# Performance work log

Hardware: AMD Instinct MI355X
Metric: run time of the kernel (lower is better)

The kernel has to match this reference:

```python
import jax, jax.numpy as jnp
import numpy as np

# dims from init_kwargs
B, T = 64, 128
CB, DB = 8, 256
IN_DIM = CB + DB            # 264
H_STATE = 512
NUM_HEADS = 4
NUM_SHIFT = 3
M = 128                     # memory content size (slot width)
A = 2048                    # number of memory addresses
READ_SIZE = NUM_HEADS * M   # 512
PARAMS_PER_HEAD = M + 1 + 1 + NUM_SHIFT + 1 + 2 * M  # key,beta,g,shift,gamma,erase,add = 390
UPDATE_SIZE = NUM_HEADS * PARAMS_PER_HEAD             # 1560
EPS = 1e-8


def setup_inputs() -> dict:
    key = jax.random.key(0)
    ks = jax.random.split(key, 4)
    w = lambda k, sh: jax.random.normal(k, sh, jnp.float32) * 0.02
    return {
        "x": jax.random.normal(ks[0], (B, T, IN_DIM), jnp.float32),
        "W_state": w(ks[1], (IN_DIM + H_STATE + READ_SIZE, H_STATE)),
        "b_state": jnp.zeros((H_STATE,), jnp.float32),
        "W_out": w(ks[2], (H_STATE, DB)),
        "b_out": jnp.zeros((DB,), jnp.float32),
        "W_upd": w(ks[3], (H_STATE, UPDATE_SIZE)),
        "b_upd": jnp.zeros((UPDATE_SIZE,), jnp.float32),
    }


def _ntm_step(params, carry, x_t):
    W_state, b_state, W_out, b_out, W_upd, b_upd = params
    h, wt, mem = carry  # h [B,S], wt [B,H,A], mem [B,M,A]

    # --- read from memory with previous attention ---
    read = jnp.einsum('bma,bha->bhm', mem, wt).reshape(B, READ_SIZE)

    # --- controller ---
    ctrl_in = jnp.concatenate([x_t, h, read], axis=-1)
    h_new = jax.nn.sigmoid(ctrl_in @ W_state + b_state)
    out = jax.nn.sigmoid(h_new @ W_out + b_out)
    upd = (h_new @ W_upd + b_upd).reshape(B, NUM_HEADS, PARAMS_PER_HEAD)

    # --- split interface parameters per head ---
    k_vec = upd[..., :M]                                              # key [B,H,M]
    beta = jax.nn.softplus(upd[..., M:M + 1])                         # key strength
    g = jax.nn.sigmoid(upd[..., M + 1:M + 2])                         # interpolation gate
    shift = jax.nn.softmax(upd[..., M + 2:M + 2 + NUM_SHIFT], axis=-1)
    gamma = 1.0 + jax.nn.softplus(upd[..., M + 2 + NUM_SHIFT:M + 3 + NUM_SHIFT])
    erase = jax.nn.sigmoid(upd[..., M + 3 + NUM_SHIFT:2 * M + 3 + NUM_SHIFT])
    add = jnp.tanh(upd[..., 2 * M + 3 + NUM_SHIFT:])

    # --- content addressing: cosine similarity + sharpened softmax ---
    dots = jnp.einsum('bhm,bma->bha', k_vec, mem)
    k_norm = jnp.linalg.norm(k_vec, axis=-1, keepdims=True)           # [B,H,1]
    m_norm = jnp.linalg.norm(mem, axis=1)[:, None, :]                 # [B,1,A]
    sim = dots / (k_norm * m_norm + EPS)
    wc = jax.nn.softmax(beta * sim, axis=-1)

    # --- gate with previous attention ---
    wg = g * wc + (1.0 - g) * wt

    # --- circular convolutional shift (small fixed loop over NUM_SHIFT) ---
    center = NUM_SHIFT // 2
    shifted = jnp.stack([jnp.roll(wg, s - center, axis=-1) for s in range(NUM_SHIFT)], axis=2)  # [B,H,S,A]
    ws = jnp.einsum('bhs,bhsa->bha', shift, shifted)

    # --- sharpening ---
    wp = jnp.power(ws + EPS, gamma)
    wt_new = wp / jnp.sum(wp, axis=-1, keepdims=True)

    # --- memory erase / add ---
    erase_term = jnp.prod(1.0 - jnp.einsum('bhm,bha->bhma', erase, wt_new), axis=1)  # [B,M,A]
    add_term = jnp.einsum('bhm,bha->bma', add, wt_new)
    mem_new = mem * erase_term + add_term

    return (h_new, wt_new, mem_new), out


def reference(x, W_state, b_state, W_out, b_out, W_upd, b_upd):
    # init_state (matches torch module): h=ones, wt one-hot at address 0, mem=0.01
    h0 = jnp.ones((B, H_STATE), jnp.float32)
    wt0 = jnp.zeros((B, NUM_HEADS, A), jnp.float32).at[:, :, 0].set(1.0)
    mem0 = jnp.full((B, M, A), 0.01, jnp.float32)
    params = (W_state, b_state, W_out, b_out, W_upd, b_upd)

    def step(carry, x_t):
        return _ntm_step(params, carry, x_t)

    _, outs = jax.lax.scan(step, (h0, wt0, mem0), jnp.swapaxes(x, 0, 1))
    return jnp.swapaxes(outs, 0, 1)  # [B, T, DB]
```

## Files before the change

kernel.cpp:

```cpp
#include <hip/hip_runtime.h>
#include <math.h>

#define BB 64
#define TT 128
#define DBX 256
#define IND 264
#define HS 512
#define NH 4
#define MMM 128
#define AAA 2048
#define PPH 390
#define NCOLS (DBX + NH*PPH)
#define KTOT (IND + HS + HS)
#define KSPL 8
#define KCH  161
#define EPSF 1e-8f

__device__ __forceinline__ float sigmf(float x){ return 1.0f/(1.0f+expf(-x)); }
__device__ __forceinline__ float softplusf(float x){ return (x > 20.0f) ? x : log1pf(expf(x)); }

__global__ void k_init(float* __restrict__ hT, float* __restrict__ readT,
                       float* __restrict__ wt, float* __restrict__ mem){
  int i = blockIdx.x*blockDim.x + threadIdx.x;
  int stride = gridDim.x*blockDim.x;
  for (int idx=i; idx<BB*MMM*AAA; idx+=stride) mem[idx]=0.01f;
  for (int idx=i; idx<HS*BB; idx+=stride){ hT[idx]=1.0f; readT[idx]=0.01f; }
  for (int idx=i; idx<BB*NH*AAA; idx+=stride) wt[idx] = ((idx & (AAA-1))==0)?1.0f:0.0f;
}

__global__ __launch_bounds__(256) void k_tx(const float* __restrict__ x, float* __restrict__ xT){
  int b = blockIdx.x;
  for (int f = threadIdx.x; f < TT*IND; f += 256)
    xT[(size_t)f*BB + b] = x[(size_t)b*TT*IND + f];
}

__global__ __launch_bounds__(256) void k1_state(
    const float* __restrict__ xT, const float* __restrict__ Wst,
    const float* __restrict__ hTp, const float* __restrict__ readTp,
    float* __restrict__ hpart, float* __restrict__ wcsum, float* __restrict__ wpsum, int t)
{
  int tid = threadIdx.x, wave = tid>>6, lane = tid&63;
  int ks = blockIdx.y;
  int j0 = blockIdx.x*16 + wave*4;
  if (blockIdx.x==0 && ks==0){
    wcsum[tid] = 0.0f;
    wpsum[tid] = 0.0f;
  }
  float a0=0,a1=0,a2=0,a3=0;
  int k0 = ks*KCH, kend = k0+KCH;

  #define K1STEP(AEXPR) { float aV=(AEXPR); \
      float4 wv = *(const float4*)(Wst + (size_t)k*HS + j0); \
      a0 += aV*wv.x; a1 += aV*wv.y; a2 += aV*wv.z; a3 += aV*wv.w; }

  {int s = k0, e = kend<IND?kend:IND;
   #pragma unroll 4
   for (int k=s;k<e;++k) K1STEP(xT[((size_t)t*IND + k)*BB + lane]); }
  {int s = k0>IND?k0:IND, e = kend<(IND+HS)?kend:(IND+HS);
   #pragma unroll 4
   for (int k=s;k<e;++k) K1STEP(hTp[(k-IND)*BB + lane]); }
  {int s = k0>(IND+HS)?k0:(IND+HS), e = kend;
   #pragma unroll 4
   for (int k=s;k<e;++k) K1STEP(readTp[(k-IND-HS)*BB + lane]); }
  #undef K1STEP

  float* hp = hpart + (size_t)ks*HS*BB + (size_t)j0*BB + lane;
  hp[0]    = a0;
  hp[BB]   = a1;
  hp[2*BB] = a2;
  hp[3*BB] = a3;
}

__global__ __launch_bounds__(512) void k2h(
    const float* __restrict__ hpart, const float* __restrict__ bst, float* __restrict__ hTn)
{
  int idx = blockIdx.x*512 + threadIdx.x;
  float v = 0.0f;
  #pragma unroll
  for (int ks=0; ks<KSPL; ++ks) v += hpart[(size_t)ks*HS*BB + idx];
  hTn[idx] = sigmf(v + bst[idx>>6]);
}

__global__ __launch_bounds__(256) void k2_outupd(
    const float* __restrict__ hTn,
    const float* __restrict__ Wout, const float* __restrict__ bout,
    const float* __restrict__ Wupd, const float* __restrict__ bupd,
    float* __restrict__ out,
    float* __restrict__ kvec_t, float* __restrict__ beta, float* __restrict__ gbuf,
    float* __restrict__ gam, float* __restrict__ shraw,
    float* __restrict__ erase, float* __restrict__ addb, int t)
{
  __shared__ float part[4][8][BB];
  int tid = threadIdx.x, ks = tid>>6, lane = tid&63;
  int c0 = blockIdx.x*8;
  bool isout = (c0 < DBX);
  size_t strd = isout ? (size_t)DBX : (size_t)(NH*PPH);
  const float* wbase = isout ? (Wout + c0) : (Wupd + (c0 - DBX));
  bool valid = (c0 < NCOLS);

  float acc[8] = {0,0,0,0,0,0,0,0};
  if (valid){
    int k0 = ks*128;
    #pragma unroll 4
    for (int k=k0; k<k0+128; ++k){
      float a = hTn[k*BB + lane];
      const float4* w4 = (const float4*)(wbase + (size_t)k*strd);
      float4 wa = w4[0], wb = w4[1];
      acc[0]+=a*wa.x; acc[1]+=a*wa.y; acc[2]+=a*wa.z; acc[3]+=a*wa.w;
      acc[4]+=a*wb.x; acc[5]+=a*wb.y; acc[6]+=a*wb.z; acc[7]+=a*wb.w;
    }
  }
  #pragma unroll
  for (int u=0; u<8; ++u) part[ks][u][lane] = acc[u];
  __syncthreads();
  if (!valid) return;

  for (int idx=tid; idx<8*BB; idx+=256){
    int u = idx>>6, b = idx&63;
    int c = c0+u;
    float v = part[0][u][b] + part[1][u][b] + part[2][u][b] + part[3][u][b];
    if (isout){
      out[((size_t)b*TT + t)*DBX + c] = sigmf(v + bout[c]);
    } else {
      int u2 = c - DBX;
      int hh = u2 / PPH;
      int p  = u2 - hh*PPH;
      v += bupd[u2];
      if (p < MMM)            kvec_t[b*HS + p*NH + hh] = v;
      else if (p == MMM)      beta[b*NH+hh] = softplusf(v);
      else if (p == MMM+1)    gbuf[b*NH+hh] = sigmf(v);
      else if (p <  MMM+5)    shraw[(b*NH+hh)*3 + (p-(MMM+2))] = v;
      else if (p == MMM+5)    gam[b*NH+hh] = 1.0f + softplusf(v);
      else if (p <  2*MMM+6)  erase[b*HS + hh*MMM + (p-(MMM+6))] = sigmf(v);
      else                    addb[b*HS + hh*MMM + (p-(2*MMM+6))] = tanhf(v);
    }
  }
}

__global__ __launch_bounds__(512) void k_dotsP(
    const float* __restrict__ mem, const float* __restrict__ kvec_t,
    float* __restrict__ dpart, float* __restrict__ n2part)
{
  int b = blockIdx.x, s = blockIdx.y, z = blockIdx.z, tid = threadIdx.x;
  __shared__ __align__(16) float klt[128];
  if (tid < 128) klt[tid] = kvec_t[b*HS + z*128 + tid];
  __syncthreads();
  int a = s*512 + tid;
  const float* mp = mem + (size_t)b*MMM*AAA + (size_t)(z*32)*AAA + a;
  const float4* k4 = (const float4*)klt;
  float a0=0,a1=0,a2=0,a3=0,n2=0;
  #pragma unroll 8
  for (int m=0; m<32; ++m){
    float mv = mp[(size_t)m*AAA];
    float4 kv = k4[m];
    a0 += kv.x*mv; a1 += kv.y*mv; a2 += kv.z*mv; a3 += kv.w*mv;
    n2 += mv*mv;
  }
  size_t base = ((size_t)(z*BB+b)*NH)*AAA + a;
  dpart[base]        = a0;
  dpart[base+AAA]    = a1;
  dpart[base+2*AAA]  = a2;
  dpart[base+3*AAA]  = a3;
  n2part[(size_t)(z*BB+b)*AAA + a] = n2;
}

__global__ __launch_bounds__(512) void k_dotsF(
    const float* __restrict__ dpart, const float* __restrict__ n2part,
    const float* __restrict__ kvec_t, const float* __restrict__ beta,
    float* __restrict__ ebuf, float* __restrict__ wcsum)
{
  int b = blockIdx.x, s = blockIdx.y, tid = threadIdx.x;
  __shared__ float red[HS];
  __shared__ float kn[NH];
  __shared__ float rsum[8*NH];
  float kv = kvec_t[b*HS + tid];
  red[tid] = kv*kv;
  __syncthreads();
  #pragma unroll
  for (int off=256; off>=4; off>>=1){
    if (tid < off) red[tid] += red[tid+off];
    __syncthreads();
  }
  if (tid < NH) kn[tid] = sqrtf(red[tid]);
  __syncthreads();

  int a = s*512 + tid;
  float d[NH] = {0,0,0,0};
  float n2 = 0.0f;
  #pragma unroll
  for (int z=0; z<4; ++z){
    size_t base = ((size_t)(z*BB+b)*NH)*AAA + a;
    d[0] += dpart[base];
    d[1] += dpart[base+AAA];
    d[2] += dpart[base+2*AAA];
    d[3] += dpart[base+3*AAA];
    n2   += n2part[(size_t)(z*BB+b)*AAA + a];
  }
  float mn = sqrtf(n2);
  int wid = tid >> 6, lane = tid & 63;
  #pragma unroll
  for (int hh=0; hh<NH; ++hh){
    float sim = d[hh]/(kn[hh]*mn + EPSF);
    float e = expf(beta[b*NH+hh]*sim);
    ebuf[((size_t)(b*NH+hh))*AAA + a] = e;
    float v = e;
    #pragma unroll
    for (int off=32; off>0; off>>=1) v += __shfl_xor(v, off);
    if (lane==0) rsum[wid*NH+hh] = v;
  }
  __syncthreads();
  if (tid < NH){
    float s2 = 0.0f;
    #pragma unroll
    for (int w=0; w<8; ++w) s2 += rsum[w*NH+tid];
    atomicAdd(&wcsum[b*NH+tid], s2);
  }
}

__global__ __launch_bounds__(512) void k_shift(
    const float* __restrict__ ebuf, const float* __restrict__ wcsum,
    const float* __restrict__ gbuf, const float* __restrict__ shraw,
    const float* __restrict__ gam, const float* __restrict__ wt,
    float* __restrict__ wpb, float* __restrict__ wpsum)
{
  int b = blockIdx.x, s = blockIdx.y, tid = threadIdx.x;
  int a = s*512 + tid;
  int am1 = (a + AAA - 1) & (AAA-1);
  int ap1 = (a + 1) & (AAA-1);
  __shared__ float sh[NH*3], gl[NH], gml[NH], winv[NH];
  __shared__ float rsum[8*NH];
  if (tid < NH){
    int hh = tid;
    float s0=shraw[(b*NH+hh)*3], s1=shraw[(b*NH+hh)*3+1], s2=shraw[(b*NH+hh)*3+2];
    float mx = fmaxf(s0, fmaxf(s1, s2));
    float e0=expf(s0-mx), e1=expf(s1-mx), e2=expf(s2-mx);
    float inv = 1.0f/(e0+e1+e2);
    sh[hh*3+0]=e0*inv; sh[hh*3+1]=e1*inv; sh[hh*3+2]=e2*inv;
    gl[hh]  = gbuf[b*NH+hh];
    gml[hh] = gam[b*NH+hh];
    winv[hh]= 1.0f/wcsum[b*NH+hh];
  }
  __syncthreads();
  int wid = tid >> 6, lane = tid & 63;
  #pragma unroll
  for (int hh=0; hh<NH; ++hh){
    const float* eb = ebuf + ((size_t)(b*NH+hh))*AAA;
    const float* wb = wt   + ((size_t)(b*NH+hh))*AAA;
    float inv = winv[hh], g = gl[hh];
    float s0 = sh[hh*3+0], s1 = sh[hh*3+1], s2 = sh[hh*3+2];
    float wgm1 = g*eb[am1]*inv + (1.0f-g)*wb[am1];
    float wg0  = g*eb[a]  *inv + (1.0f-g)*wb[a];
    float wgp1 = g*eb[ap1]*inv + (1.0f-g)*wb[ap1];
    float ws = s0*wgp1 + s1*wg0 + s2*wgm1;
    float wp = powf(ws + EPSF, gml[hh]);
    wpb[((size_t)(b*NH+hh))*AAA + a] = wp;
    float v = wp;
    #pragma unroll
    for (int off=32; off>0; off>>=1) v += __shfl_xor(v, off);
    if (lane==0) rsum[wid*NH+hh] = v;
  }
  __syncthreads();
  if (tid < NH){
    float s3 = 0.0f;
    #pragma unroll
    for (int w=0; w<8; ++w) s3 += rsum[w*NH+tid];
    atomicAdd(&wpsum[b*NH+tid], s3);
  }
}

__global__ __launch_bounds__(512) void k_updA(
    float* __restrict__ mem, const float* __restrict__ wpb, const float* __restrict__ wpsum,
    const float* __restrict__ erase, const float* __restrict__ addb,
    float* __restrict__ wt)
{
  int b = blockIdx.x, s = blockIdx.y, z = blockIdx.z, tid = threadIdx.x;
  int a = s*512 + tid;
  __shared__ __align__(16) float ert[128];
  __shared__ __align__(16) float adt[128];
  if (tid < 128){
    int m = tid >> 2, hh = tid & 3;
    ert[tid] = erase[b*HS + hh*MMM + z*32 + m];
    adt[tid] = addb [b*HS + hh*MMM + z*32 + m];
  }
  float wtn[NH];
  #pragma unroll
  for (int hh=0; hh<NH; ++hh){
    float w = wpb[((size_t)(b*NH+hh))*AAA + a] / wpsum[b*NH+hh];
    wtn[hh] = w;
    if (z == 0) wt[((size_t)(b*NH+hh))*AAA + a] = w;
  }
  __syncthreads();

  float* mp = mem + (size_t)b*MMM*AAA + (size_t)(z*32)*AAA + a;
  const float4* e4 = (const float4*)ert;
  const float4* a4 = (const float4*)adt;
  #pragma unroll 8
  for (int m=0; m<32; ++m){
    float mv = mp[(size_t)m*AAA];
    float4 ev = e4[m], av = a4[m];
    float et = (1.0f - ev.x*wtn[0]) * (1.0f - ev.y*wtn[1])
             * (1.0f - ev.z*wtn[2]) * (1.0f - ev.w*wtn[3]);
    float at = av.x*wtn[0] + av.y*wtn[1] + av.z*wtn[2] + av.w*wtn[3];
    mp[(size_t)m*AAA] = mv*et + at;
  }
}

__global__ __launch_bounds__(512) void k_updB(
    const float* __restrict__ mem, const float* __restrict__ wt,
    float* __restrict__ readTn)
{
  int b = blockIdx.x, my = blockIdx.y, tid = threadIdx.x;
  int wave = tid >> 6, lane = tid & 63;
  int m0 = my*8 + wave;
  int m1 = m0 + 64;
  const float* row0 = mem + (size_t)b*MMM*AAA + (size_t)m0*AAA;
  const float* row1 = mem + (size_t)b*MMM*AAA + (size_t)m1*AAA;
  const float* w0 = wt + ((size_t)(b*NH+0))*AAA;
  const float* w1 = wt + ((size_t)(b*NH+1))*AAA;
  const float* w2 = wt + ((size_t)(b*NH+2))*AAA;
  const float* w3 = wt + ((size_t)(b*NH+3))*AAA;
  float r00=0,r01=0,r02=0,r03=0, r10=0,r11=0,r12=0,r13=0;
  #pragma unroll 4
  for (int it=0; it<32; ++it){
    int a = it*64 + lane;
    float mv0 = row0[a], mv1 = row1[a];
    float wv0 = w0[a], wv1 = w1[a], wv2 = w2[a], wv3 = w3[a];
    r00 += mv0*wv0; r01 += mv0*wv1; r02 += mv0*wv2; r03 += mv0*wv3;
    r10 += mv1*wv0; r11 += mv1*wv1; r12 += mv1*wv2; r13 += mv1*wv3;
  }
  float rr[2][NH] = {{r00,r01,r02,r03},{r10,r11,r12,r13}};
  #pragma unroll
  for (int q=0; q<2; ++q){
    #pragma unroll
    for (int hh=0; hh<NH; ++hh){
      float v = rr[q][hh];
      #pragma unroll
      for (int off=32; off>0; off>>=1) v += __shfl_xor(v, off);
      rr[q][hh] = v;
    }
  }
  if (lane == 0){
    #pragma unroll
    for (int hh=0; hh<NH; ++hh){
      readTn[(size_t)(hh*MMM+m0)*BB + b] = rr[0][hh];
      readTn[(size_t)(hh*MMM+m1)*BB + b] = rr[1][hh];
    }
  }
}

extern "C" void kernel_launch(void* const* d_in, const int* in_sizes, int n_in,
                              void* d_out, int out_size, void* d_ws, size_t ws_size,
                              hipStream_t stream){
  const float* x    = (const float*)d_in[0];
  const float* Wst  = (const float*)d_in[1];
  const float* bst  = (const float*)d_in[2];
  const float* Wout = (const float*)d_in[3];
  const float* bout = (const float*)d_in[4];
  const float* Wupd = (const float*)d_in[5];
  const float* bupd = (const float*)d_in[6];
  float* out = (float*)d_out;

  float* p = (float*)d_ws;
  float* hT     = p; p += 2*HS*BB;
  float* readT  = p; p += 2*HS*BB;
  float* hpart  = p; p += KSPL*HS*BB;
  float* xT     = p; p += (size_t)TT*IND*BB;
  float* wt     = p; p += BB*NH*AAA;
  float* mem    = p; p += (size_t)BB*MMM*AAA;
  float* kvec_t = p; p += BB*HS;
  float* beta   = p; p += BB*NH;
  float* gbuf   = p; p += BB*NH;
  float* gam    = p; p += BB*NH;
  float* shraw  = p; p += BB*NH*3;
  float* erase  = p; p += BB*HS;
  float* addb   = p; p += BB*HS;
  float* ebuf   = p; p += BB*NH*AAA;
  float* wpb    = p; p += 4*BB*NH*AAA;
  float* n2part = p; p += 4*BB*AAA;
  float* wcsum  = p; p += BB*NH;
  float* wpsum  = p; p += BB*NH;
  float* dpart  = wpb;

  k_init<<<2048, 256, 0, stream>>>(hT, readT, wt, mem);
  k_tx<<<BB, 256, 0, stream>>>(x, xT);
  for (int t=0; t<TT; ++t){
    const float* hTp = hT    + (t&1)*HS*BB;
    float* hTn       = hT    + ((t+1)&1)*HS*BB;
    const float* rTp = readT + (t&1)*HS*BB;
    float* rTn       = readT + ((t+1)&1)*HS*BB;
    k1_state<<<dim3(32,KSPL), 256, 0, stream>>>(xT, Wst, hTp, rTp, hpart, wcsum, wpsum, t);
    k2h<<<64, 512, 0, stream>>>(hpart, bst, hTn);
    k2_outupd<<<dim3(259), 256, 0, stream>>>(hTn, Wout, bout, Wupd, bupd, out,
        kvec_t, beta, gbuf, gam, shraw, erase, addb, t);
    k_dotsP<<<dim3(BB,4,4), 512, 0, stream>>>(mem, kvec_t, dpart, n2part);
    k_dotsF<<<dim3(BB,4), 512, 0, stream>>>(dpart, n2part, kvec_t, beta, ebuf, wcsum);
    k_shift<<<dim3(BB,4), 512, 0, stream>>>(ebuf, wcsum, gbuf, shraw, gam, wt, wpb, wpsum);
    k_updA<<<dim3(BB,4,4), 512, 0, stream>>>(mem, wpb, wpsum, erase, addb, wt);
    k_updB<<<dim3(BB,8), 512, 0, stream>>>(mem, wt, rTn);
  }
}
```

Measured before the change: 11.57 ms.

## Fuse memory read into the memory update kernel using LDS and atomics

Merges the memory erase/add update kernel with the following read kernel. Each block stages the freshly updated memory tile and the normalized attention weights in shared memory, computes partial per-head dot products, and accumulates them into the read buffer with atomics. The read buffer is zeroed inside the shift kernel. This removes one kernel launch per timestep and a second full pass over the 64x128x2048 memory, in exchange for extra barriers, about 24KB of LDS per block, and atomic contention on the read outputs.

```diff
diff --git a/kernel.cpp b/kernel.cpp
--- a/kernel.cpp
+++ b/kernel.cpp
@@ -221,7 +221,7 @@
     const float* __restrict__ ebuf, const float* __restrict__ wcsum,
     const float* __restrict__ gbuf, const float* __restrict__ shraw,
     const float* __restrict__ gam, const float* __restrict__ wt,
-    float* __restrict__ wpb, float* __restrict__ wpsum)
+    float* __restrict__ wpb, float* __restrict__ wpsum, float* __restrict__ readTn)
 {
   int b = blockIdx.x, s = blockIdx.y, tid = threadIdx.x;
   int a = s*512 + tid;
@@ -229,6 +229,7 @@
   int ap1 = (a + 1) & (AAA-1);
   __shared__ float sh[NH*3], gl[NH], gml[NH], winv[NH];
   __shared__ float rsum[8*NH];
+  if (s == 0) readTn[(size_t)tid*BB + b] = 0.0f;
   if (tid < NH){
     int hh = tid;
     float s0=shraw[(b*NH+hh)*3], s1=shraw[(b*NH+hh)*3+1], s2=shraw[(b*NH+hh)*3+2];
@@ -268,15 +269,17 @@
   }
 }
 
-__global__ __launch_bounds__(512) void k_updA(
+__global__ __launch_bounds__(512) void k_updAB(
     float* __restrict__ mem, const float* __restrict__ wpb, const float* __restrict__ wpsum,
     const float* __restrict__ erase, const float* __restrict__ addb,
-    float* __restrict__ wt)
+    float* __restrict__ wt, float* __restrict__ readTn)
 {
   int b = blockIdx.x, s = blockIdx.y, z = blockIdx.z, tid = threadIdx.x;
   int a = s*512 + tid;
   __shared__ __align__(16) float ert[128];
   __shared__ __align__(16) float adt[128];
+  __shared__ float wtT[NH][512];
+  __shared__ float ldsM[8][512];
   if (tid < 128){
     int m = tid >> 2, hh = tid & 3;
     ert[tid] = erase[b*HS + hh*MMM + z*32 + m];
@@ -287,6 +290,7 @@
   for (int hh=0; hh<NH; ++hh){
     float w = wpb[((size_t)(b*NH+hh))*AAA + a] / wpsum[b*NH+hh];
     wtn[hh] = w;
+    wtT[hh][tid] = w;
     if (z == 0) wt[((size_t)(b*NH+hh))*AAA + a] = w;
   }
   __syncthreads();
@@ -294,56 +298,46 @@
   float* mp = mem + (size_t)b*MMM*AAA + (size_t)(z*32)*AAA + a;
   const float4* e4 = (const float4*)ert;
   const float4* a4 = (const float4*)adt;
-  #pragma unroll 8
-  for (int m=0; m<32; ++m){
-    float mv = mp[(size_t)m*AAA];
-    float4 ev = e4[m], av = a4[m];
-    float et = (1.0f - ev.x*wtn[0]) * (1.0f - ev.y*wtn[1])
-             * (1.0f - ev.z*wtn[2]) * (1.0f - ev.w*wtn[3]);
-    float at = av.x*wtn[0] + av.y*wtn[1] + av.z*wtn[2] + av.w*wtn[3];
-    mp[(size_t)m*AAA] = mv*et + at;
-  }
-}
-
-__global__ __launch_bounds__(512) void k_updB(
-    const float* __restrict__ mem, const float* __restrict__ wt,
-    float* __restrict__ readTn)
-{
-  int b = blockIdx.x, my = blockIdx.y, tid = threadIdx.x;
-  int wave = tid >> 6, lane = tid & 63;
-  int m0 = my*8 + wave;
-  int m1 = m0 + 64;
-  const float* row0 = mem + (size_t)b*MMM*AAA + (size_t)m0*AAA;
-  const float* row1 = mem + (size_t)b*MMM*AAA + (size_t)m1*AAA;
-  const float* w0 = wt + ((size_t)(b*NH+0))*AAA;
-  const float* w1 = wt + ((size_t)(b*NH+1))*AAA;
-  const float* w2 = wt + ((size_t)(b*NH+2))*AAA;
-  const float* w3 = wt + ((size_t)(b*NH+3))*AAA;
-  float r00=0,r01=0,r02=0,r03=0, r10=0,r11=0,r12=0,r13=0;
-  #pragma unroll 4
-  for (int it=0; it<32; ++it){
-    int a = it*64 + lane;
-    float mv0 = row0[a], mv1 = row1[a];
-    float wv0 = w0[a], wv1 = w1[a], wv2 = w2[a], wv3 = w3[a];
-    r00 += mv0*wv0; r01 += mv0*wv1; r02 += mv0*wv2; r03 += mv0*wv3;
-    r10 += mv1*wv0; r11 += mv1*wv1; r12 += mv1*wv2; r13 += mv1*wv3;
-  }
-  float rr[2][NH] = {{r00,r01,r02,r03},{r10,r11,r12,r13}};
-  #pragma unroll
-  for (int q=0; q<2; ++q){
+  int lane = tid & 63, wave = tid >> 6;
+
+  for (int q4=0; q4<4; ++q4){
+    if (q4) __syncthreads();
+    #pragma unroll 8
+    for (int mloc=0; mloc<8; ++mloc){
+      int m = q4*8 + mloc;
+      float mv = mp[(size_t)m*AAA];
+      float4 ev = e4[m], av = a4[m];
+      float et = (1.0f - ev.x*wtn[0]) * (1.0f - ev.y*wtn[1])
+               * (1.0f - ev.z*wtn[2]) * (1.0f - ev.w*wtn[3]);
+      float at = av.x*wtn[0] + av.y*wtn[1] + av.z*wtn[2] + av.w*wtn[3];
+      float mnv = mv*et + at;
+      mp[(size_t)m*AAA] = mnv;
+      ldsM[mloc][tid] = mnv;
+    }
+    __syncthreads();
+    float r0=0,r1=0,r2=0,r3=0;
+    #pragma unroll
+    for (int q=0; q<8; ++q){
+      int col = lane + 64*q;
+      float mvv = ldsM[wave][col];
+      r0 += mvv*wtT[0][col];
+      r1 += mvv*wtT[1][col];
+      r2 += mvv*wtT[2][col];
+      r3 += mvv*wtT[3][col];
+    }
+    float rr[NH] = {r0,r1,r2,r3};
     #pragma unroll
     for (int hh=0; hh<NH; ++hh){
-      float v = rr[q][hh];
+      float v = rr[hh];
       #pragma unroll
       for (int off=32; off>0; off>>=1) v += __shfl_xor(v, off);
-      rr[q][hh] = v;
-    }
-  }
-  if (lane == 0){
-    #pragma unroll
-    for (int hh=0; hh<NH; ++hh){
-      readTn[(size_t)(hh*MMM+m0)*BB + b] = rr[0][hh];
-      readTn[(size_t)(hh*MMM+m1)*BB + b] = rr[1][hh];
+      rr[hh] = v;
+    }
+    if (lane == 0){
+      int m = z*32 + q4*8 + wave;
+      #pragma unroll
+      for (int hh=0; hh<NH; ++hh)
+        atomicAdd(&readTn[(size_t)(hh*MMM+m)*BB + b], rr[hh]);
     }
   }
 }
@@ -394,8 +388,7 @@
         kvec_t, beta, gbuf, gam, shraw, erase, addb, t);
     k_dotsP<<<dim3(BB,4,4), 512, 0, stream>>>(mem, kvec_t, dpart, n2part);
     k_dotsF<<<dim3(BB,4), 512, 0, stream>>>(dpart, n2part, kvec_t, beta, ebuf, wcsum);
-    k_shift<<<dim3(BB,4), 512, 0, stream>>>(ebuf, wcsum, gbuf, shraw, gam, wt, wpb, wpsum);
-    k_updA<<<dim3(BB,4,4), 512, 0, stream>>>(mem, wpb, wpsum, erase, addb, wt);
-    k_updB<<<dim3(BB,8), 512, 0, stream>>>(mem, wt, rTn);
-  }
-}
+    k_shift<<<dim3(BB,4), 512, 0, stream>>>(ebuf, wcsum, gbuf, shraw, gam, wt, wpb, wpsum, rTn);
+    k_updAB<<<dim3(BB,4,4), 512, 0, stream>>>(mem, wpb, wpsum, erase, addb, wt, rTn);
+  }
+}
```

Result: slower. 12.41 ms (+7.2%).

## Fuse memory erase/add update with next-step read into one kernel

Applied to the files above, without the earlier changes.

Merges the memory update kernel and the memory read kernel so each memory row is loaded once, updated, written back, and immediately dotted with the new attention weights. The normalized weights for all four heads are staged in 32 KB of shared memory per block. This removes one full read pass over the 64 MB memory tensor and one launch per timestep. In exchange, grid parallelism drops from 1024 to 512 blocks, and the large shared-memory footprint may limit occupancy.

```diff
diff --git a/kernel.cpp b/kernel.cpp
--- a/kernel.cpp
+++ b/kernel.cpp
@@ -268,65 +268,64 @@
   }
 }
 
-__global__ __launch_bounds__(512) void k_updA(
+__global__ __launch_bounds__(512) void k_updAB(
     float* __restrict__ mem, const float* __restrict__ wpb, const float* __restrict__ wpsum,
     const float* __restrict__ erase, const float* __restrict__ addb,
-    float* __restrict__ wt)
-{
-  int b = blockIdx.x, s = blockIdx.y, z = blockIdx.z, tid = threadIdx.x;
-  int a = s*512 + tid;
-  __shared__ __align__(16) float ert[128];
-  __shared__ __align__(16) float adt[128];
-  if (tid < 128){
-    int m = tid >> 2, hh = tid & 3;
-    ert[tid] = erase[b*HS + hh*MMM + z*32 + m];
-    adt[tid] = addb [b*HS + hh*MMM + z*32 + m];
-  }
-  float wtn[NH];
-  #pragma unroll
-  for (int hh=0; hh<NH; ++hh){
-    float w = wpb[((size_t)(b*NH+hh))*AAA + a] / wpsum[b*NH+hh];
-    wtn[hh] = w;
-    if (z == 0) wt[((size_t)(b*NH+hh))*AAA + a] = w;
-  }
-  __syncthreads();
-
-  float* mp = mem + (size_t)b*MMM*AAA + (size_t)(z*32)*AAA + a;
-  const float4* e4 = (const float4*)ert;
-  const float4* a4 = (const float4*)adt;
-  #pragma unroll 8
-  for (int m=0; m<32; ++m){
-    float mv = mp[(size_t)m*AAA];
-    float4 ev = e4[m], av = a4[m];
-    float et = (1.0f - ev.x*wtn[0]) * (1.0f - ev.y*wtn[1])
-             * (1.0f - ev.z*wtn[2]) * (1.0f - ev.w*wtn[3]);
-    float at = av.x*wtn[0] + av.y*wtn[1] + av.z*wtn[2] + av.w*wtn[3];
-    mp[(size_t)m*AAA] = mv*et + at;
-  }
-}
-
-__global__ __launch_bounds__(512) void k_updB(
-    const float* __restrict__ mem, const float* __restrict__ wt,
-    float* __restrict__ readTn)
-{
+    float* __restrict__ wt, float* __restrict__ readTn)
+{
+  __shared__ __align__(16) float wl[AAA*4];
   int b = blockIdx.x, my = blockIdx.y, tid = threadIdx.x;
   int wave = tid >> 6, lane = tid & 63;
-  int m0 = my*8 + wave;
-  int m1 = m0 + 64;
-  const float* row0 = mem + (size_t)b*MMM*AAA + (size_t)m0*AAA;
-  const float* row1 = mem + (size_t)b*MMM*AAA + (size_t)m1*AAA;
-  const float* w0 = wt + ((size_t)(b*NH+0))*AAA;
-  const float* w1 = wt + ((size_t)(b*NH+1))*AAA;
-  const float* w2 = wt + ((size_t)(b*NH+2))*AAA;
-  const float* w3 = wt + ((size_t)(b*NH+3))*AAA;
+  float winv[4];
+  #pragma unroll
+  for (int h=0;h<4;++h) winv[h] = 1.0f/wpsum[b*NH+h];
+  #pragma unroll
+  for (int c4=0;c4<4;++c4){
+    int a = c4*512 + tid;
+    float w0 = wpb[((size_t)(b*NH+0))*AAA + a]*winv[0];
+    float w1 = wpb[((size_t)(b*NH+1))*AAA + a]*winv[1];
+    float w2 = wpb[((size_t)(b*NH+2))*AAA + a]*winv[2];
+    float w3 = wpb[((size_t)(b*NH+3))*AAA + a]*winv[3];
+    wl[a*4+0]=w0; wl[a*4+1]=w1; wl[a*4+2]=w2; wl[a*4+3]=w3;
+    if (my == 0){
+      wt[((size_t)(b*NH+0))*AAA + a] = w0;
+      wt[((size_t)(b*NH+1))*AAA + a] = w1;
+      wt[((size_t)(b*NH+2))*AAA + a] = w2;
+      wt[((size_t)(b*NH+3))*AAA + a] = w3;
+    }
+  }
+  __syncthreads();
+
+  int m0 = my*8 + wave, m1 = m0 + 64;
+  float er0[4], ad0[4], er1[4], ad1[4];
+  #pragma unroll
+  for (int h=0;h<4;++h){
+    er0[h] = erase[b*HS + h*MMM + m0];
+    ad0[h] = addb [b*HS + h*MMM + m0];
+    er1[h] = erase[b*HS + h*MMM + m1];
+    ad1[h] = addb [b*HS + h*MMM + m1];
+  }
+  float* row0 = mem + (size_t)b*MMM*AAA + (size_t)m0*AAA;
+  float* row1 = mem + (size_t)b*MMM*AAA + (size_t)m1*AAA;
+  const float4* wl4 = (const float4*)wl;
   float r00=0,r01=0,r02=0,r03=0, r10=0,r11=0,r12=0,r13=0;
   #pragma unroll 4
   for (int it=0; it<32; ++it){
     int a = it*64 + lane;
     float mv0 = row0[a], mv1 = row1[a];
-    float wv0 = w0[a], wv1 = w1[a], wv2 = w2[a], wv3 = w3[a];
-    r00 += mv0*wv0; r01 += mv0*wv1; r02 += mv0*wv2; r03 += mv0*wv3;
-    r10 += mv1*wv0; r11 += mv1*wv1; r12 += mv1*wv2; r13 += mv1*wv3;
+    float4 w4 = wl4[a];
+    float et0 = (1.0f - er0[0]*w4.x)*(1.0f - er0[1]*w4.y)
+              * (1.0f - er0[2]*w4.z)*(1.0f - er0[3]*w4.w);
+    float at0 = ad0[0]*w4.x + ad0[1]*w4.y + ad0[2]*w4.z + ad0[3]*w4.w;
+    float n0 = mv0*et0 + at0;
+    row0[a] = n0;
+    r00 += n0*w4.x; r01 += n0*w4.y; r02 += n0*w4.z; r03 += n0*w4.w;
+    float et1 = (1.0f - er1[0]*w4.x)*(1.0f - er1[1]*w4.y)
+              * (1.0f - er1[2]*w4.z)*(1.0f - er1[3]*w4.w);
+    float at1 = ad1[0]*w4.x + ad1[1]*w4.y + ad1[2]*w4.z + ad1[3]*w4.w;
+    float n1 = mv1*et1 + at1;
+    row1[a] = n1;
+    r10 += n1*w4.x; r11 += n1*w4.y; r12 += n1*w4.z; r13 += n1*w4.w;
   }
   float rr[2][NH] = {{r00,r01,r02,r03},{r10,r11,r12,r13}};
   #pragma unroll
@@ -375,7 +374,7 @@
   float* erase  = p; p += BB*HS;
   float* addb   = p; p += BB*HS;
   float* ebuf   = p; p += BB*NH*AAA;
-  float* wpb    = p; p += 4*BB*NH*AAA;
+  float* wpb    = p; p += 4*(size_t)BB*NH*AAA;
   float* n2part = p; p += 4*BB*AAA;
   float* wcsum  = p; p += BB*NH;
   float* wpsum  = p; p += BB*NH;
@@ -395,7 +394,6 @@
     k_dotsP<<<dim3(BB,4,4), 512, 0, stream>>>(mem, kvec_t, dpart, n2part);
     k_dotsF<<<dim3(BB,4), 512, 0, stream>>>(dpart, n2part, kvec_t, beta, ebuf, wcsum);
     k_shift<<<dim3(BB,4), 512, 0, stream>>>(ebuf, wcsum, gbuf, shraw, gam, wt, wpb, wpsum);
-    k_updA<<<dim3(BB,4,4), 512, 0, stream>>>(mem, wpb, wpsum, erase, addb, wt);
-    k_updB<<<dim3(BB,8), 512, 0, stream>>>(mem, wt, rTn);
-  }
-}
+    k_updAB<<<dim3(BB,8), 512, 0, stream>>>(mem, wpb, wpsum, erase, addb, wt, rTn);
+  }
+}
```

Result: faster. 10.36 ms (-10.5%).
